# Kernel tuning notes

Hardware: AMD Instinct MI355X
Metric: run time of the kernel (lower is better)

The kernel has to match this reference:

```python
import jax, jax.numpy as jnp
import numpy as np

B, S, N, D = 1, 512, 384, 64
H, DP, DQK = 32, 128, 64
LAMBDA_INIT = 1.0
EPS = 1e-32
SCALING = DQK ** -0.5


def _layer_norm(x, g, b):
    m = jnp.mean(x, axis=-1, keepdims=True)
    v = jnp.mean(jnp.square(x - m), axis=-1, keepdims=True)
    return (x - m) * jax.lax.rsqrt(v + 1e-5) * g + b


def setup_inputs() -> dict:
    key = jax.random.key(0)
    ks = jax.random.split(key, 12)
    msa = jax.random.normal(ks[0], (B, S, N, D), dtype=jnp.float32)
    Wq = jax.random.normal(ks[1], (2 * DQK, D), dtype=jnp.float32) * 0.02
    Wk = Wq + jax.random.normal(ks[2], (2 * DQK, D), dtype=jnp.float32) * 0.1 * 0.02
    Wl = jax.random.normal(ks[3], (H, D), dtype=jnp.float32) * 0.02
    Wr = jax.random.normal(ks[4], (H, D), dtype=jnp.float32) * 0.02
    Wp = jax.random.normal(ks[5], (2 * DP, H * H), dtype=jnp.float32) * 0.02
    bp = jnp.zeros((2 * DP,), dtype=jnp.float32)
    lq1 = jax.random.normal(ks[6], (DQK,), dtype=jnp.float32) * 0.1
    lk1 = jax.random.normal(ks[7], (DQK,), dtype=jnp.float32) * 0.1
    lq2 = jax.random.normal(ks[8], (DQK,), dtype=jnp.float32) * 0.1
    lk2 = jax.random.normal(ks[9], (DQK,), dtype=jnp.float32) * 0.1
    return {
        'msa': msa,
        'ln_g': jnp.ones((D,), jnp.float32), 'ln_b': jnp.zeros((D,), jnp.float32),
        'Wq': Wq, 'Wk': Wk,
        'qn_g': jnp.ones((DQK,), jnp.float32), 'qn_b': jnp.zeros((DQK,), jnp.float32),
        'kn_g': jnp.ones((DQK,), jnp.float32), 'kn_b': jnp.zeros((DQK,), jnp.float32),
        'lq1': lq1, 'lk1': lk1, 'lq2': lq2, 'lk2': lk2,
        'Wl': Wl, 'Wr': Wr, 'Wp': Wp, 'bp': bp,
    }


def reference(msa, ln_g, ln_b, Wq, Wk, qn_g, qn_b, kn_g, kn_b,
              lq1, lk1, lq2, lk2, Wl, Wr, Wp, bp):
    b, s, n, d = msa.shape
    x = _layer_norm(msa, ln_g, ln_b)  # [b,s,n,d]

    # differential sequence attention (all masks are all-True by default)
    q = (x[:, 0] @ Wq.T).reshape(b, n, 2, DQK).transpose(0, 2, 1, 3)       # [b,2,n,dqk]
    k = (x @ Wk.T).reshape(b, s, n, 2, DQK).transpose(0, 3, 1, 2, 4)       # [b,2,s,n,dqk]
    q = _layer_norm(q, qn_g, qn_b)
    k = _layer_norm(k, kn_g, kn_b)
    sw = jnp.einsum('btnd,btsnd->btsn', q, k) * SCALING                     # [b,2,s,n]
    sw = sw.sum(axis=-1) / (n + EPS)                                        # [b,2,s]
    lam = jnp.exp(jnp.sum(lq1 * lk1)) - jnp.exp(jnp.sum(lq2 * lk2)) + LAMBDA_INIT
    sw = sw[:, 0] - lam * sw[:, 1]                                          # [b,s]
    seq_weights = jax.nn.softmax(sw, axis=-1)                               # [b,s]

    # weighted left/right hidden projections
    a = jnp.einsum('bsnd,hd->bnsh', x, Wl)
    bt = jnp.einsum('bsnd,hd->bnsh', x, Wr)
    ws = jnp.sqrt(seq_weights + EPS)[:, None, :, None]                      # [b,1,s,1]
    a = a * ws
    bt = bt * ws

    # outer product mean over sequences, then pairwise projection + SwiGLU
    outer = jnp.einsum('bisc,bjse->bijce', a, bt).reshape(b, n, n, H * H)   # [b,n,n,h^2]
    out = outer @ Wp.T + bp                                                 # [b,n,n,2*dp]
    val, gate = jnp.split(out, 2, axis=-1)
    return jax.nn.silu(gate) * val                                          # [b,n,n,dp]
```

## Files before the change

kernel.cpp:

```cpp
#include <hip/hip_runtime.h>
#include <hip/hip_bf16.h>
#include <math.h>

#define WS_X        0u
#define WS_AEXT     12582912u
#define WS_BEXT     18874368u
#define WS_QG       25165824u
#define WS_SQG      25214976u
#define WS_SQB      25215744u
#define WS_PART     25216512u
#define WS_WSQ      25219584u
#define WS_BPP      25220096u
#define WS_WPF      25220352u

typedef __attribute__((ext_vector_type(8))) short bf16x8;
typedef __attribute__((ext_vector_type(4))) float f32x4;

union U4B8 { uint4 u4; unsigned u[4]; bf16x8 v; };

__device__ __forceinline__ unsigned short f2b(float x) {
    __hip_bfloat16 b = __float2bfloat16(x);
    return *reinterpret_cast<unsigned short*>(&b);
}
__device__ __forceinline__ float b2f(unsigned short u) {
    __hip_bfloat16 b = *reinterpret_cast<__hip_bfloat16*>(&u);
    return __bfloat162float(b);
}

#define GLDS(g, l) __builtin_amdgcn_global_load_lds(                                   \
    (const __attribute__((address_space(1))) unsigned int*)(g),                        \
    (__attribute__((address_space(3))) unsigned int*)(l), 16, 0, 0)

__global__ __launch_bounds__(256) void k1_ln(const float* __restrict__ msa,
                                             const float* __restrict__ g,
                                             const float* __restrict__ bb,
                                             float* __restrict__ x) {
    int row = blockIdx.x * 16 + (threadIdx.x >> 4);
    int l16 = threadIdx.x & 15;
    float4 v = ((const float4*)msa)[(size_t)row * 16 + l16];
    float sum = v.x + v.y + v.z + v.w;
    #pragma unroll
    for (int m = 1; m < 16; m <<= 1) sum += __shfl_xor(sum, m);
    float mean = sum * (1.0f / 64.0f);
    float4 dv = make_float4(v.x - mean, v.y - mean, v.z - mean, v.w - mean);
    float sq = dv.x * dv.x + dv.y * dv.y + dv.z * dv.z + dv.w * dv.w;
    #pragma unroll
    for (int m = 1; m < 16; m <<= 1) sq += __shfl_xor(sq, m);
    float r = rsqrtf(sq * (1.0f / 64.0f) + 1e-5f);
    float4 g4 = ((const float4*)g)[l16];
    float4 b4 = ((const float4*)bb)[l16];
    ((float4*)x)[(size_t)row * 16 + l16] = make_float4(
        dv.x * r * g4.x + b4.x, dv.y * r * g4.y + b4.y,
        dv.z * r * g4.z + b4.z, dv.w * r * g4.w + b4.w);
}

__global__ __launch_bounds__(128) void k2_q(const float* __restrict__ x,
                                            const float* __restrict__ Wq,
                                            const float* __restrict__ qg_,
                                            const float* __restrict__ qb_,
                                            const float* __restrict__ kg_,
                                            const float* __restrict__ kb_,
                                            float* __restrict__ qgOut,
                                            float* __restrict__ SqgOut,
                                            float* __restrict__ SqbOut) {
    int n = blockIdx.x;
    int tt = threadIdx.x >> 6;
    int d = threadIdx.x & 63;
    const float* xr = x + (size_t)n * 64;
    const float* w  = Wq + (size_t)(tt * 64 + d) * 64;
    float acc = 0.f;
    #pragma unroll 8
    for (int dd = 0; dd < 64; ++dd) acc += xr[dd] * w[dd];
    float sum = acc;
    #pragma unroll
    for (int m = 1; m < 64; m <<= 1) sum += __shfl_xor(sum, m);
    float mean = sum * (1.0f / 64.0f);
    float dv = acc - mean;
    float sq = dv * dv;
    #pragma unroll
    for (int m = 1; m < 64; m <<= 1) sq += __shfl_xor(sq, m);
    float r = rsqrtf(sq * (1.0f / 64.0f) + 1e-5f);
    float qnv = dv * r * qg_[d] + qb_[d];
    float qgv = qnv * kg_[d];
    float sb  = qnv * kb_[d];
    float sg  = qgv;
    #pragma unroll
    for (int m = 1; m < 64; m <<= 1) { sg += __shfl_xor(sg, m); sb += __shfl_xor(sb, m); }
    qgOut[(size_t)(tt * 384 + n) * 64 + d] = qgv;
    if (d == 0) { SqgOut[tt * 384 + n] = sg; SqbOut[tt * 384 + n] = sb; }
}

__global__ __launch_bounds__(256) void gemm_k3(const float* __restrict__ X,
                                               const float* __restrict__ Wk,
                                               const float* __restrict__ qg,
                                               const float* __restrict__ Sqg,
                                               const float* __restrict__ Sqb,
                                               float* __restrict__ part) {
    __shared__ __align__(16) char smem[65536];
    float (*AsT)[132] = (float(*)[132])smem;
    float (*BsT)[132] = (float(*)[132])(smem + 16896);
    float* kbuf = (float*)smem;

    int t  = threadIdx.x;
    int m0 = blockIdx.x * 128;
    int s  = m0 / 384;
    int nchunk = (m0 - s * 384) >> 7;
    int tr = t >> 4, tc = t & 15;
    float acc[8][8] = {};
    int rrow = t >> 3;
    int kk   = (t & 7) * 4;
    for (int k0 = 0; k0 < 64; k0 += 32) {
        #pragma unroll
        for (int l = 0; l < 4; ++l) {
            int row = rrow + 32 * l;
            float4 va = *(const float4*)(X + (size_t)(m0 + row) * 64 + k0 + kk);
            AsT[kk + 0][row] = va.x; AsT[kk + 1][row] = va.y;
            AsT[kk + 2][row] = va.z; AsT[kk + 3][row] = va.w;
            float4 vb = *(const float4*)(Wk + (size_t)row * 64 + k0 + kk);
            BsT[kk + 0][row] = vb.x; BsT[kk + 1][row] = vb.y;
            BsT[kk + 2][row] = vb.z; BsT[kk + 3][row] = vb.w;
        }
        __syncthreads();
        #pragma unroll 4
        for (int k = 0; k < 32; ++k) {
            float a[8], b[8];
            *(float4*)&a[0] = *(const float4*)&AsT[k][tr * 8];
            *(float4*)&a[4] = *(const float4*)&AsT[k][tr * 8 + 4];
            *(float4*)&b[0] = *(const float4*)&BsT[k][tc * 8];
            *(float4*)&b[4] = *(const float4*)&BsT[k][tc * 8 + 4];
            #pragma unroll
            for (int q = 0; q < 8; ++q)
                #pragma unroll
                for (int j = 0; j < 8; ++j)
                    acc[q][j] += a[q] * b[j];
        }
        __syncthreads();
    }
    #pragma unroll
    for (int q = 0; q < 8; ++q) {
        int m = tr * 8 + q;
        int swz = (m & 15) << 4;
        int b0 = m * 512 + (((tc * 2) * 16) ^ swz);
        int b1 = m * 512 + (((tc * 2 + 1) * 16) ^ swz);
        *(float4*)((char*)kbuf + b0) = make_float4(acc[q][0], acc[q][1], acc[q][2], acc[q][3]);
        *(float4*)((char*)kbuf + b1) = make_float4(acc[q][4], acc[q][5], acc[q][6], acc[q][7]);
    }
    __syncthreads();
    int r  = t & 127;
    int tt = t >> 7;
    int n  = nchunk * 128 + r;
    const char* base = (const char*)kbuf + r * 512;
    const float4* qgp = (const float4*)(qg + ((size_t)(tt * 384 + n)) * 64);
    int swz = (r & 15) << 4;
    float s1 = 0.f, s2 = 0.f, s3 = 0.f;
    #pragma unroll
    for (int i = 0; i < 16; ++i) {
        float4 kv = *(const float4*)(base + ((((tt * 16 + i) * 16) ^ swz)));
        float4 qv = qgp[i];
        s1 += kv.x + kv.y + kv.z + kv.w;
        s2 += kv.x * kv.x + kv.y * kv.y + kv.z * kv.z + kv.w * kv.w;
        s3 += kv.x * qv.x + kv.y * qv.y + kv.z * qv.z + kv.w * qv.w;
    }
    float mu  = s1 * (1.0f / 64.0f);
    float var = s2 * (1.0f / 64.0f) - mu * mu;
    float rln = rsqrtf(var + 1e-5f);
    float dot = rln * (s3 - mu * Sqg[tt * 384 + n]) + Sqb[tt * 384 + n];
    #pragma unroll
    for (int m = 1; m < 64; m <<= 1) dot += __shfl_xor(dot, m);
    __syncthreads();
    if ((t & 63) == 0) kbuf[t >> 6] = dot;
    __syncthreads();
    if (t == 0) part[((size_t)0 * 512 + s) * 3 + nchunk] = kbuf[0] + kbuf[1];
    if (t == 1) part[((size_t)1 * 512 + s) * 3 + nchunk] = kbuf[2] + kbuf[3];
}

__global__ __launch_bounds__(512) void k4_softmax(const float* __restrict__ part,
                                                  const float* __restrict__ lq1,
                                                  const float* __restrict__ lk1,
                                                  const float* __restrict__ lq2,
                                                  const float* __restrict__ lk2,
                                                  float* __restrict__ wsq) {
    int s = threadIdx.x;
    float l1 = 0.f, l2 = 0.f;
    for (int i = 0; i < 64; ++i) { l1 += lq1[i] * lk1[i]; l2 += lq2[i] * lk2[i]; }
    float lam = expf(l1) - expf(l2) + 1.0f;
    const float c = 0.125f / 384.0f;
    float a0 = (part[s * 3] + part[s * 3 + 1] + part[s * 3 + 2]) * c;
    float a1 = (part[(512 + s) * 3] + part[(512 + s) * 3 + 1] + part[(512 + s) * 3 + 2]) * c;
    float v = a0 - lam * a1;
    __shared__ float red[512];
    red[s] = v;
    __syncthreads();
    for (int off = 256; off > 0; off >>= 1) {
        if (s < off) red[s] = fmaxf(red[s], red[s + off]);
        __syncthreads();
    }
    float mx = red[0];
    __syncthreads();
    float e = expf(v - mx);
    red[s] = e;
    __syncthreads();
    for (int off = 256; off > 0; off >>= 1) {
        if (s < off) red[s] += red[s + off];
        __syncthreads();
    }
    wsq[s] = sqrtf(e / red[0] + 1e-32f);
}

__global__ __launch_bounds__(256) void k5_ab(const float* __restrict__ x,
                                             const float* __restrict__ Wl,
                                             const float* __restrict__ Wr,
                                             const float* __restrict__ wsq,
                                             unsigned short* __restrict__ AHo,
                                             unsigned short* __restrict__ ALo,
                                             unsigned short* __restrict__ BHo,
                                             unsigned short* __restrict__ BLo) {
    int i  = blockIdx.x;
    int s0 = blockIdx.y * 64;
    int t  = threadIdx.x;
    __shared__ __align__(16) float wl[2048], wr[2048];
    __shared__ float xT[64][69];
    ((float4*)wl)[t * 2]     = ((const float4*)Wl)[t * 2];
    ((float4*)wl)[t * 2 + 1] = ((const float4*)Wl)[t * 2 + 1];
    ((float4*)wr)[t * 2]     = ((const float4*)Wr)[t * 2];
    ((float4*)wr)[t * 2 + 1] = ((const float4*)Wr)[t * 2 + 1];
    {
        int s_l = t >> 2, d0 = (t & 3) * 16;
        const float* xr = x + ((size_t)(s0 + s_l) * 384 + i) * 64 + d0;
        #pragma unroll
        for (int j = 0; j < 4; ++j) {
            float4 v = *(const float4*)(xr + j * 4);
            xT[d0 + j * 4 + 0][s_l] = v.x; xT[d0 + j * 4 + 1][s_l] = v.y;
            xT[d0 + j * 4 + 2][s_l] = v.z; xT[d0 + j * 4 + 3][s_l] = v.w;
        }
    }
    __syncthreads();
    int c = t >> 3, so = (t & 7) * 8;
    float aa[8] = {}, bb2[8] = {};
    #pragma unroll 8
    for (int d = 0; d < 64; ++d) {
        float wlv = wl[c * 64 + d], wrv = wr[c * 64 + d];
        #pragma unroll
        for (int q = 0; q < 8; ++q) {
            float xv = xT[d][so + q];
            aa[q]  += xv * wlv;
            bb2[q] += xv * wrv;
        }
    }
    #pragma unroll
    for (int q = 0; q < 8; ++q) {
        float wq = wsq[s0 + so + q];
        aa[q] *= wq; bb2[q] *= wq;
    }
    int m = i * 32 + c;
    int s = s0 + so;
    size_t idx = (((size_t)(m >> 4) * 16 + (s >> 5)) * 64 + ((m & 15) | (((s >> 3) & 3) << 4))) * 8;
    {
        unsigned short h[8], l[8];
        #pragma unroll
        for (int q = 0; q < 8; ++q) { h[q] = f2b(aa[q]); l[q] = f2b(aa[q] - b2f(h[q])); }
        *(uint4*)&AHo[idx] = make_uint4((unsigned)h[0] | ((unsigned)h[1] << 16), (unsigned)h[2] | ((unsigned)h[3] << 16),
                                        (unsigned)h[4] | ((unsigned)h[5] << 16), (unsigned)h[6] | ((unsigned)h[7] << 16));
        *(uint4*)&ALo[idx] = make_uint4((unsigned)l[0] | ((unsigned)l[1] << 16), (unsigned)l[2] | ((unsigned)l[3] << 16),
                                        (unsigned)l[4] | ((unsigned)l[5] << 16), (unsigned)l[6] | ((unsigned)l[7] << 16));
    }
    {
        unsigned short h[8], l[8];
        #pragma unroll
        for (int q = 0; q < 8; ++q) { h[q] = f2b(bb2[q]); l[q] = f2b(bb2[q] - b2f(h[q])); }
        *(uint4*)&BHo[idx] = make_uint4((unsigned)h[0] | ((unsigned)h[1] << 16), (unsigned)h[2] | ((unsigned)h[3] << 16),
                                        (unsigned)h[4] | ((unsigned)h[5] << 16), (unsigned)h[6] | ((unsigned)h[7] << 16));
        *(uint4*)&BLo[idx] = make_uint4((unsigned)l[0] | ((unsigned)l[1] << 16), (unsigned)l[2] | ((unsigned)l[3] << 16),
                                        (unsigned)l[4] | ((unsigned)l[5] << 16), (unsigned)l[6] | ((unsigned)l[7] << 16));
    }
}

__global__ __launch_bounds__(256) void prep_wp(const float* __restrict__ Wp,
                                               const float* __restrict__ bp,
                                               unsigned short* __restrict__ WpF,
                                               float* __restrict__ bpP) {
    int gid = blockIdx.x * 256 + threadIdx.x;
    int lane  = gid & 63;
    int kstep = (gid >> 6) & 31;
    int nb    = (gid >> 11) & 15;
    int bsel  = gid >> 15;
    int rl = lane & 15, kg = lane >> 4;
    int urow = nb * 16 + rl;
    int srow = (urow & 1) ? 128 + (urow >> 1) : (urow >> 1);
    int k0 = kstep * 32 + kg * 8;
    const float* src = Wp + (size_t)srow * 1024 + k0;
    unsigned short o[8];
    #pragma unroll
    for (int e = 0; e < 8; ++e) {
        float w = src[e];
        unsigned short h = f2b(w);
        o[e] = bsel ? f2b(w - b2f(h)) : h;
    }
    *(uint4*)&WpF[(size_t)gid * 8] = make_uint4(
        (unsigned)o[0] | ((unsigned)o[1] << 16), (unsigned)o[2] | ((unsigned)o[3] << 16),
        (unsigned)o[4] | ((unsigned)o[5] << 16), (unsigned)o[6] | ((unsigned)o[7] << 16));
    if (blockIdx.x == 0) {
        int tt = threadIdx.x;
        bpP[tt] = bp[(tt & 1) ? 128 + (tt >> 1) : (tt >> 1)];
    }
}

__global__ __launch_bounds__(256) void gemm_fused(const unsigned short* __restrict__ AH,
                                                  const unsigned short* __restrict__ AL,
                                                  const unsigned short* __restrict__ BHm,
                                                  const unsigned short* __restrict__ BLm,
                                                  const unsigned short* __restrict__ WpF,
                                                  const float* __restrict__ bpP,
                                                  float* __restrict__ out) {
    __shared__ __align__(16) unsigned char smem[65536];
    unsigned* pa = (unsigned*)smem;

    const int t = threadIdx.x;
    const int wave = t >> 6, lane = t & 63;
    const int bx = blockIdx.x, by = blockIdx.y;
    const int m0 = bx * 128, n0 = by * 128;
    const int wm = (wave & 1) * 64, wn = (wave >> 1) * 64;
    const int kgrp = lane >> 4, rl = lane & 15;
    f32x4 acc[4][4] = {};

    const unsigned short* srcArr = (wave == 0) ? AH : (wave == 1) ? AL : (wave == 2) ? BHm : BLm;
    const unsigned short* srcBase = srcArr + ((size_t)(((wave < 2) ? m0 : n0) >> 4) * 16) * 512 + lane * 8;
    unsigned short* dstW = (unsigned short*)smem + wave * 4096;

    #pragma unroll
    for (int pane = 0; pane < 8; ++pane)
        GLDS(srcBase + (size_t)pane * 8192, dstW + pane * 512);

    #pragma unroll 2
    for (int kt = 0; kt < 16; ++kt) {
        if (kt < 15) {
            unsigned short* dst = dstW + ((kt + 1) & 1) * 16384;
            const unsigned short* s2 = srcBase + (size_t)(kt + 1) * 512;
            #pragma unroll
            for (int pane = 0; pane < 8; ++pane)
                GLDS(s2 + (size_t)pane * 8192, dst + pane * 512);
            asm volatile("s_waitcnt vmcnt(8)" ::: "memory");
        } else {
            asm volatile("s_waitcnt vmcnt(0)" ::: "memory");
        }
        __builtin_amdgcn_s_barrier();
        asm volatile("" ::: "memory");
        const int cb = (kt & 1) * 32768;
        bf16x8 aHf[4], aLf[4], bHf[4], bLf[4];
        #pragma unroll
        for (int f = 0; f < 4; ++f) {
            const int pA = ((wm >> 4) + f) * 1024;
            aHf[f] = *(const bf16x8*)(smem + cb + pA + lane * 16);
            aLf[f] = *(const bf16x8*)(smem + cb + 8192 + pA + lane * 16);
            const int pB = ((wn >> 4) + f) * 1024;
            bHf[f] = *(const bf16x8*)(smem + cb + 16384 + pB + lane * 16);
            bLf[f] = *(const bf16x8*)(smem + cb + 24576 + pB + lane * 16);
        }
        __builtin_amdgcn_s_setprio(1);
        #pragma unroll
        for (int mf = 0; mf < 4; ++mf)
            #pragma unroll
            for (int nf = 0; nf < 4; ++nf) {
                acc[mf][nf] = __builtin_amdgcn_mfma_f32_16x16x32_bf16(aHf[mf], bHf[nf], acc[mf][nf], 0, 0, 0);
                acc[mf][nf] = __builtin_amdgcn_mfma_f32_16x16x32_bf16(aLf[mf], bHf[nf], acc[mf][nf], 0, 0, 0);
                acc[mf][nf] = __builtin_amdgcn_mfma_f32_16x16x32_bf16(aHf[mf], bLf[nf], acc[mf][nf], 0, 0, 0);
            }
        __builtin_amdgcn_s_setprio(0);
        asm volatile("" ::: "memory");
        __builtin_amdgcn_s_barrier();
        asm volatile("" ::: "memory");
    }

    #pragma unroll
    for (int mf = 0; mf < 4; ++mf) {
        #pragma unroll
        for (int nf = 0; nf < 4; ++nf) {
            #pragma unroll
            for (int r = 0; r < 4; ++r) {
                int mloc = wm + mf * 16 + kgrp * 4 + r;
                int nloc = wn + nf * 16 + rl;
                int p = ((mloc >> 5) << 2) | (nloc >> 5);
                int k = ((mloc & 31) << 5) | (nloc & 31);
                float v = acc[mf][nf][r];
                unsigned short h = f2b(v);
                unsigned short l = f2b(v - b2f(h));
                pa[(p << 10) + (k ^ ((p & 3) << 3))] = (unsigned)h | ((unsigned)l << 16);
            }
        }
    }
    __syncthreads();

    f32x4 acc2[4] = {};
    const unsigned* paRow = pa + (rl << 10);
    const int kg8 = kgrp * 8;
    #pragma unroll 4
    for (int ks = 0; ks < 32; ++ks) {
        U4B8 ua0, ua1, aHf, aLf;
        int kb = (ks * 32 + kg8) ^ ((rl & 3) << 3);
        ua0.u4 = *(const uint4*)(paRow + kb);
        ua1.u4 = *(const uint4*)(paRow + kb + 4);
        aHf.u[0] = __builtin_amdgcn_perm(ua0.u[1], ua0.u[0], 0x05040100u);
        aHf.u[1] = __builtin_amdgcn_perm(ua0.u[3], ua0.u[2], 0x05040100u);
        aHf.u[2] = __builtin_amdgcn_perm(ua1.u[1], ua1.u[0], 0x05040100u);
        aHf.u[3] = __builtin_amdgcn_perm(ua1.u[3], ua1.u[2], 0x05040100u);
        aLf.u[0] = __builtin_amdgcn_perm(ua0.u[1], ua0.u[0], 0x07060302u);
        aLf.u[1] = __builtin_amdgcn_perm(ua0.u[3], ua0.u[2], 0x07060302u);
        aLf.u[2] = __builtin_amdgcn_perm(ua1.u[1], ua1.u[0], 0x07060302u);
        aLf.u[3] = __builtin_amdgcn_perm(ua1.u[3], ua1.u[2], 0x07060302u);
        bf16x8 bHf[4], bLf[4];
        #pragma unroll
        for (int nf = 0; nf < 4; ++nf) {
            const int nb = wave * 4 + nf;
            bHf[nf] = *(const bf16x8*)&WpF[(size_t)((nb * 32 + ks) * 64 + lane) * 8];
            bLf[nf] = *(const bf16x8*)&WpF[(size_t)(((16 + nb) * 32 + ks) * 64 + lane) * 8];
        }
        __builtin_amdgcn_s_setprio(1);
        #pragma unroll
        for (int nf = 0; nf < 4; ++nf) {
            acc2[nf] = __builtin_amdgcn_mfma_f32_16x16x32_bf16(aHf.v, bHf[nf], acc2[nf], 0, 0, 0);
            acc2[nf] = __builtin_amdgcn_mfma_f32_16x16x32_bf16(aLf.v, bHf[nf], acc2[nf], 0, 0, 0);
            acc2[nf] = __builtin_amdgcn_mfma_f32_16x16x32_bf16(aHf.v, bLf[nf], acc2[nf], 0, 0, 0);
        }
        __builtin_amdgcn_s_setprio(0);
    }

    const int parity = rl & 1;
    #pragma unroll
    for (int nf = 0; nf < 4; ++nf) {
        const int np = wave * 64 + nf * 16 + rl;
        const float bias = bpP[np];
        const int ocol = np >> 1;
        #pragma unroll
        for (int r = 0; r < 4; ++r) {
            float own = acc2[nf][r] + bias;
            float oth = __shfl_xor(own, 1);
            float v = parity ? oth : own;
            float g = parity ? own : oth;
            float res = v * (g / (1.0f + expf(-g)));
            if (parity == (r >> 1)) {
                int p = kgrp * 4 + r;
                int i = bx * 4 + (p >> 2);
                int j = by * 4 + (p & 3);
                out[((size_t)i * 384 + j) * 128 + ocol] = res;
            }
        }
    }
}

extern "C" void kernel_launch(void* const* d_in, const int* in_sizes, int n_in,
                              void* d_out, int out_size, void* d_ws, size_t ws_size,
                              hipStream_t stream) {
    const float* msa  = (const float*)d_in[0];
    const float* ln_g = (const float*)d_in[1];
    const float* ln_b = (const float*)d_in[2];
    const float* Wq   = (const float*)d_in[3];
    const float* Wk   = (const float*)d_in[4];
    const float* qn_g = (const float*)d_in[5];
    const float* qn_b = (const float*)d_in[6];
    const float* kn_g = (const float*)d_in[7];
    const float* kn_b = (const float*)d_in[8];
    const float* lq1  = (const float*)d_in[9];
    const float* lk1  = (const float*)d_in[10];
    const float* lq2  = (const float*)d_in[11];
    const float* lk2  = (const float*)d_in[12];
    const float* Wl   = (const float*)d_in[13];
    const float* Wr   = (const float*)d_in[14];
    const float* Wp   = (const float*)d_in[15];
    const float* bp   = (const float*)d_in[16];
    float* out = (float*)d_out;
    float* ws  = (float*)d_ws;

    float* x = ws + WS_X;
    unsigned short* AHs = (unsigned short*)(ws + WS_AEXT);
    unsigned short* ALs = (unsigned short*)(ws + WS_AEXT + 3145728u);
    unsigned short* BHs = (unsigned short*)(ws + WS_BEXT);
    unsigned short* BLs = (unsigned short*)(ws + WS_BEXT + 3145728u);
    float* qg   = ws + WS_QG;
    float* Sqg  = ws + WS_SQG;
    float* Sqb  = ws + WS_SQB;
    float* part = ws + WS_PART;
    float* wsq  = ws + WS_WSQ;
    float* bpP  = ws + WS_BPP;
    unsigned short* WpF = (unsigned short*)(ws + WS_WPF);

    prep_wp<<<256, 256, 0, stream>>>(Wp, bp, WpF, bpP);
    k1_ln<<<12288, 256, 0, stream>>>(msa, ln_g, ln_b, x);
    k2_q<<<384, 128, 0, stream>>>(x, Wq, qn_g, qn_b, kn_g, kn_b, qg, Sqg, Sqb);
    gemm_k3<<<1536, 256, 0, stream>>>(x, Wk, qg, Sqg, Sqb, part);
    k4_softmax<<<1, 512, 0, stream>>>(part, lq1, lk1, lq2, lk2, wsq);
    k5_ab<<<dim3(384, 8), 256, 0, stream>>>(x, Wl, Wr, wsq, AHs, ALs, BHs, BLs);
    gemm_fused<<<dim3(96, 96), 256, 0, stream>>>(AHs, ALs, BHs, BLs, WpF, bpP, out);
}
```

Measured before the change: 857.5 us.

## Enlarge fused GEMM tile to 256x256 with 8 waves and staged epilogue

```diff
diff --git a/kernel.cpp b/kernel.cpp
--- a/kernel.cpp
+++ b/kernel.cpp
@@ -305,145 +305,143 @@
     }
 }
 
-__global__ __launch_bounds__(256) void gemm_fused(const unsigned short* __restrict__ AH,
-                                                  const unsigned short* __restrict__ AL,
-                                                  const unsigned short* __restrict__ BHm,
-                                                  const unsigned short* __restrict__ BLm,
-                                                  const unsigned short* __restrict__ WpF,
-                                                  const float* __restrict__ bpP,
-                                                  float* __restrict__ out) {
-    __shared__ __align__(16) unsigned char smem[65536];
+__global__ __launch_bounds__(512, 2) void gemm_fused(const unsigned short* __restrict__ AH,
+                                                     const unsigned short* __restrict__ AL,
+                                                     const unsigned short* __restrict__ BHm,
+                                                     const unsigned short* __restrict__ BLm,
+                                                     const unsigned short* __restrict__ WpF,
+                                                     const float* __restrict__ bpP,
+                                                     float* __restrict__ out) {
+    __shared__ __align__(16) unsigned char smem[131072];
     unsigned* pa = (unsigned*)smem;
 
     const int t = threadIdx.x;
     const int wave = t >> 6, lane = t & 63;
     const int bx = blockIdx.x, by = blockIdx.y;
-    const int m0 = bx * 128, n0 = by * 128;
-    const int wm = (wave & 1) * 64, wn = (wave >> 1) * 64;
+    const int m0 = bx * 256, n0 = by * 256;
+    const int wr = wave & 3;
+    const int wc = wave >> 2;
     const int kgrp = lane >> 4, rl = lane & 15;
-    f32x4 acc[4][4] = {};
-
-    const unsigned short* srcArr = (wave == 0) ? AH : (wave == 1) ? AL : (wave == 2) ? BHm : BLm;
-    const unsigned short* srcBase = srcArr + ((size_t)(((wave < 2) ? m0 : n0) >> 4) * 16) * 512 + lane * 8;
-    unsigned short* dstW = (unsigned short*)smem + wave * 4096;
-
-    #pragma unroll
-    for (int pane = 0; pane < 8; ++pane)
-        GLDS(srcBase + (size_t)pane * 8192, dstW + pane * 512);
-
-    #pragma unroll 2
+    f32x4 acc[4][8] = {};
+
+    const unsigned short* srcArr = (wave < 2) ? AH : (wave < 4) ? AL : (wave < 6) ? BHm : BLm;
+    const int pbase = (((wave < 4) ? m0 : n0) >> 4) + (wave & 1) * 8;
+    const unsigned short* srcBase = srcArr + (size_t)pbase * 8192 + lane * 8;
+    unsigned short* dstW = (unsigned short*)smem + (wave >> 1) * 8192 + (wave & 1) * 4096;
+
+    #pragma unroll
+    for (int p = 0; p < 8; ++p)
+        GLDS(srcBase + (size_t)p * 8192, dstW + p * 512);
+
     for (int kt = 0; kt < 16; ++kt) {
         if (kt < 15) {
-            unsigned short* dst = dstW + ((kt + 1) & 1) * 16384;
+            unsigned short* dst = dstW + ((kt + 1) & 1) * 32768;
             const unsigned short* s2 = srcBase + (size_t)(kt + 1) * 512;
             #pragma unroll
-            for (int pane = 0; pane < 8; ++pane)
-                GLDS(s2 + (size_t)pane * 8192, dst + pane * 512);
+            for (int p = 0; p < 8; ++p)
+                GLDS(s2 + (size_t)p * 8192, dst + p * 512);
             asm volatile("s_waitcnt vmcnt(8)" ::: "memory");
         } else {
             asm volatile("s_waitcnt vmcnt(0)" ::: "memory");
         }
         __builtin_amdgcn_s_barrier();
         asm volatile("" ::: "memory");
-        const int cb = (kt & 1) * 32768;
-        bf16x8 aHf[4], aLf[4], bHf[4], bLf[4];
-        #pragma unroll
-        for (int f = 0; f < 4; ++f) {
-            const int pA = ((wm >> 4) + f) * 1024;
-            aHf[f] = *(const bf16x8*)(smem + cb + pA + lane * 16);
-            aLf[f] = *(const bf16x8*)(smem + cb + 8192 + pA + lane * 16);
-            const int pB = ((wn >> 4) + f) * 1024;
-            bHf[f] = *(const bf16x8*)(smem + cb + 16384 + pB + lane * 16);
-            bLf[f] = *(const bf16x8*)(smem + cb + 24576 + pB + lane * 16);
+        const int cb = (kt & 1) * 65536;
+        bf16x8 aHf[4], aLf[4];
+        #pragma unroll
+        for (int mf = 0; mf < 4; ++mf) {
+            const int pA = (wr * 4 + mf) * 1024;
+            aHf[mf] = *(const bf16x8*)(smem + cb + pA + lane * 16);
+            aLf[mf] = *(const bf16x8*)(smem + cb + 16384 + pA + lane * 16);
         }
         __builtin_amdgcn_s_setprio(1);
         #pragma unroll
-        for (int mf = 0; mf < 4; ++mf)
-            #pragma unroll
-            for (int nf = 0; nf < 4; ++nf) {
-                acc[mf][nf] = __builtin_amdgcn_mfma_f32_16x16x32_bf16(aHf[mf], bHf[nf], acc[mf][nf], 0, 0, 0);
-                acc[mf][nf] = __builtin_amdgcn_mfma_f32_16x16x32_bf16(aLf[mf], bHf[nf], acc[mf][nf], 0, 0, 0);
-                acc[mf][nf] = __builtin_amdgcn_mfma_f32_16x16x32_bf16(aHf[mf], bLf[nf], acc[mf][nf], 0, 0, 0);
+        for (int nf = 0; nf < 8; ++nf) {
+            const int pB = (wc * 8 + nf) * 1024;
+            bf16x8 bHf = *(const bf16x8*)(smem + cb + 32768 + pB + lane * 16);
+            bf16x8 bLf = *(const bf16x8*)(smem + cb + 49152 + pB + lane * 16);
+            #pragma unroll
+            for (int mf = 0; mf < 4; ++mf) {
+                acc[mf][nf] = __builtin_amdgcn_mfma_f32_16x16x32_bf16(aHf[mf], bHf, acc[mf][nf], 0, 0, 0);
+                acc[mf][nf] = __builtin_amdgcn_mfma_f32_16x16x32_bf16(aLf[mf], bHf, acc[mf][nf], 0, 0, 0);
+                acc[mf][nf] = __builtin_amdgcn_mfma_f32_16x16x32_bf16(aHf[mf], bLf, acc[mf][nf], 0, 0, 0);
             }
+        }
         __builtin_amdgcn_s_setprio(0);
         asm volatile("" ::: "memory");
         __builtin_amdgcn_s_barrier();
         asm volatile("" ::: "memory");
     }
 
-    #pragma unroll
-    for (int mf = 0; mf < 4; ++mf) {
-        #pragma unroll
-        for (int nf = 0; nf < 4; ++nf) {
+    for (int g = 0; g < 4; ++g) {
+        if (wr == g) {
+            #pragma unroll
+            for (int mf = 0; mf < 4; ++mf)
+                #pragma unroll
+                for (int nf = 0; nf < 8; ++nf) {
+                    int pl = ((mf >> 1) << 3) + wc * 4 + (nf >> 1);
+                    #pragma unroll
+                    for (int r = 0; r < 4; ++r) {
+                        int k = (((mf & 1) * 16 + kgrp * 4 + r) << 5) | ((nf & 1) * 16 + rl);
+                        float v = acc[mf][nf][r];
+                        unsigned short h = f2b(v);
+                        unsigned short l = f2b(v - b2f(h));
+                        pa[(pl << 10) + (k ^ ((pl & 3) << 3))] = (unsigned)h | ((unsigned)l << 16);
+                    }
+                }
+        }
+        __syncthreads();
+
+        f32x4 acc2[2] = {};
+        const unsigned* paRow = pa + (rl << 10);
+        const int kg8 = kgrp * 8;
+        #pragma unroll 4
+        for (int ks = 0; ks < 32; ++ks) {
+            U4B8 ua0, ua1, aHf, aLf;
+            int kb = (ks * 32 + kg8) ^ ((rl & 3) << 3);
+            ua0.u4 = *(const uint4*)(paRow + kb);
+            ua1.u4 = *(const uint4*)(paRow + kb + 4);
+            aHf.u[0] = __builtin_amdgcn_perm(ua0.u[1], ua0.u[0], 0x05040100u);
+            aHf.u[1] = __builtin_amdgcn_perm(ua0.u[3], ua0.u[2], 0x05040100u);
+            aHf.u[2] = __builtin_amdgcn_perm(ua1.u[1], ua1.u[0], 0x05040100u);
+            aHf.u[3] = __builtin_amdgcn_perm(ua1.u[3], ua1.u[2], 0x05040100u);
+            aLf.u[0] = __builtin_amdgcn_perm(ua0.u[1], ua0.u[0], 0x07060302u);
+            aLf.u[1] = __builtin_amdgcn_perm(ua0.u[3], ua0.u[2], 0x07060302u);
+            aLf.u[2] = __builtin_amdgcn_perm(ua1.u[1], ua1.u[0], 0x07060302u);
+            aLf.u[3] = __builtin_amdgcn_perm(ua1.u[3], ua1.u[2], 0x07060302u);
+            #pragma unroll
+            for (int nf2 = 0; nf2 < 2; ++nf2) {
+                const int nb = wave * 2 + nf2;
+                bf16x8 bHf = *(const bf16x8*)&WpF[(size_t)((nb * 32 + ks) * 64 + lane) * 8];
+                bf16x8 bLf = *(const bf16x8*)&WpF[(size_t)(((16 + nb) * 32 + ks) * 64 + lane) * 8];
+                acc2[nf2] = __builtin_amdgcn_mfma_f32_16x16x32_bf16(aHf.v, bHf, acc2[nf2], 0, 0, 0);
+                acc2[nf2] = __builtin_amdgcn_mfma_f32_16x16x32_bf16(aLf.v, bHf, acc2[nf2], 0, 0, 0);
+                acc2[nf2] = __builtin_amdgcn_mfma_f32_16x16x32_bf16(aHf.v, bLf, acc2[nf2], 0, 0, 0);
+            }
+        }
+
+        const int parity = rl & 1;
+        #pragma unroll
+        for (int nf2 = 0; nf2 < 2; ++nf2) {
+            const int np = wave * 32 + nf2 * 16 + rl;
+            const float bias = bpP[np];
+            const int ocol = np >> 1;
             #pragma unroll
             for (int r = 0; r < 4; ++r) {
-                int mloc = wm + mf * 16 + kgrp * 4 + r;
-                int nloc = wn + nf * 16 + rl;
-                int p = ((mloc >> 5) << 2) | (nloc >> 5);
-                int k = ((mloc & 31) << 5) | (nloc & 31);
-                float v = acc[mf][nf][r];
-                unsigned short h = f2b(v);
-                unsigned short l = f2b(v - b2f(h));
-                pa[(p << 10) + (k ^ ((p & 3) << 3))] = (unsigned)h | ((unsigned)l << 16);
+                float own = acc2[nf2][r] + bias;
+                float oth = __shfl_xor(own, 1);
+                float v = parity ? oth : own;
+                float gg = parity ? own : oth;
+                float res = v * (gg / (1.0f + expf(-gg)));
+                if (parity == (r >> 1)) {
+                    int pl2 = kgrp * 4 + r;
+                    int i = bx * 8 + g * 2 + (pl2 >> 3);
+                    int j = by * 8 + (pl2 & 7);
+                    out[((size_t)i * 384 + j) * 128 + ocol] = res;
+                }
             }
         }
-    }
-    __syncthreads();
-
-    f32x4 acc2[4] = {};
-    const unsigned* paRow = pa + (rl << 10);
-    const int kg8 = kgrp * 8;
-    #pragma unroll 4
-    for (int ks = 0; ks < 32; ++ks) {
-        U4B8 ua0, ua1, aHf, aLf;
-        int kb = (ks * 32 + kg8) ^ ((rl & 3) << 3);
-        ua0.u4 = *(const uint4*)(paRow + kb);
-        ua1.u4 = *(const uint4*)(paRow + kb + 4);
-        aHf.u[0] = __builtin_amdgcn_perm(ua0.u[1], ua0.u[0], 0x05040100u);
-        aHf.u[1] = __builtin_amdgcn_perm(ua0.u[3], ua0.u[2], 0x05040100u);
-        aHf.u[2] = __builtin_amdgcn_perm(ua1.u[1], ua1.u[0], 0x05040100u);
-        aHf.u[3] = __builtin_amdgcn_perm(ua1.u[3], ua1.u[2], 0x05040100u);
-        aLf.u[0] = __builtin_amdgcn_perm(ua0.u[1], ua0.u[0], 0x07060302u);
-        aLf.u[1] = __builtin_amdgcn_perm(ua0.u[3], ua0.u[2], 0x07060302u);
-        aLf.u[2] = __builtin_amdgcn_perm(ua1.u[1], ua1.u[0], 0x07060302u);
-        aLf.u[3] = __builtin_amdgcn_perm(ua1.u[3], ua1.u[2], 0x07060302u);
-        bf16x8 bHf[4], bLf[4];
-        #pragma unroll
-        for (int nf = 0; nf < 4; ++nf) {
-            const int nb = wave * 4 + nf;
-            bHf[nf] = *(const bf16x8*)&WpF[(size_t)((nb * 32 + ks) * 64 + lane) * 8];
-            bLf[nf] = *(const bf16x8*)&WpF[(size_t)(((16 + nb) * 32 + ks) * 64 + lane) * 8];
-        }
-        __builtin_amdgcn_s_setprio(1);
-        #pragma unroll
-        for (int nf = 0; nf < 4; ++nf) {
-            acc2[nf] = __builtin_amdgcn_mfma_f32_16x16x32_bf16(aHf.v, bHf[nf], acc2[nf], 0, 0, 0);
-            acc2[nf] = __builtin_amdgcn_mfma_f32_16x16x32_bf16(aLf.v, bHf[nf], acc2[nf], 0, 0, 0);
-            acc2[nf] = __builtin_amdgcn_mfma_f32_16x16x32_bf16(aHf.v, bLf[nf], acc2[nf], 0, 0, 0);
-        }
-        __builtin_amdgcn_s_setprio(0);
-    }
-
-    const int parity = rl & 1;
-    #pragma unroll
-    for (int nf = 0; nf < 4; ++nf) {
-        const int np = wave * 64 + nf * 16 + rl;
-        const float bias = bpP[np];
-        const int ocol = np >> 1;
-        #pragma unroll
-        for (int r = 0; r < 4; ++r) {
-            float own = acc2[nf][r] + bias;
-            float oth = __shfl_xor(own, 1);
-            float v = parity ? oth : own;
-            float g = parity ? own : oth;
-            float res = v * (g / (1.0f + expf(-g)));
-            if (parity == (r >> 1)) {
-                int p = kgrp * 4 + r;
-                int i = bx * 4 + (p >> 2);
-                int j = by * 4 + (p & 3);
-                out[((size_t)i * 384 + j) * 128 + ocol] = res;
-            }
-        }
+        __syncthreads();
     }
 }
 
@@ -489,5 +487,5 @@
     gemm_k3<<<1536, 256, 0, stream>>>(x, Wk, qg, Sqg, Sqb, part);
     k4_softmax<<<1, 512, 0, stream>>>(part, lq1, lk1, lq2, lk2, wsq);
     k5_ab<<<dim3(384, 8), 256, 0, stream>>>(x, Wl, Wr, wsq, AHs, ALs, BHs, BLs);
-    gemm_fused<<<dim3(96, 96), 256, 0, stream>>>(AHs, ALs, BHs, BLs, WpF, bpP, out);
-}
+    gemm_fused<<<dim3(48, 48), 512, 0, stream>>>(AHs, ALs, BHs, BLs, WpF, bpP, out);
+}
```

New measurement: 932.8 us. 8.8% more time.
